# Optimization experiments

Hardware: AMD Instinct MI355X
Metric: run time of the kernel (lower is better)

## Reference

```python
import jax, jax.numpy as jnp
import numpy as np

B, N, D, STK_TOTAL = 8, 2048, 128, 4000


def setup_inputs() -> dict:
    key = jax.random.key(0)
    k1, k2, k3, k4 = jax.random.split(key, 4)
    x = jax.random.normal(k1, (B, N, D), dtype=jnp.float32)
    stk_ten = jax.random.randint(k2, (B, N), 0, STK_TOTAL, dtype=jnp.int32)
    # learned parameter tables (trained state; original inits: ones / xavier-uniform)
    stk_matrix = jax.random.normal(k3, (STK_TOTAL, STK_TOTAL), dtype=jnp.float32)
    stk_weight = jax.random.normal(k4, (STK_TOTAL, STK_TOTAL), dtype=jnp.float32)
    return {"x": x, "stk_ten": stk_ten, "stk_matrix": stk_matrix, "stk_weight": stk_weight}


def reference(x, stk_ten, stk_matrix, stk_weight):
    # x: [B, N, D]; stk_ten: [B, N] int ids < STK_TOTAL
    idx = stk_ten.astype(jnp.int32)
    # per-batch double gather -> [B, N, N] submatrices (vectorized index_select x2)
    M = stk_matrix[idx[:, :, None], idx[:, None, :]]          # [B, N, N]
    W = jnp.abs(stk_weight[idx[:, :, None], idx[:, None, :]])  # [B, N, N]
    n = idx.shape[1]
    eye = jnp.eye(n, dtype=bool)                               # diag removal mask
    M = jnp.where(eye, jnp.float32(0.0), M)                    # stk_m_s - diag_embed(diag)
    W = jnp.where(eye, jnp.float32(0.0), W)
    # dropout is identity in inference mode (training=False)
    att = jax.nn.softmax(W, axis=2)                            # [B, N, N]
    out = jnp.matmul(M * att, x)                               # [B, N, D]
    return out
```

## Files before the change

### kernel.cpp

```cpp
#include <hip/hip_runtime.h>
#include <hip/hip_fp16.h>
#include <math.h>

#define BATCH 8
#define N 2048
#define D 128
#define ST 4000

#define TJ 64
#define IT 16
#define KQ 4
#define TPW 8

typedef short bf16x8 __attribute__((ext_vector_type(8)));
typedef float f32x4  __attribute__((ext_vector_type(4)));
typedef unsigned u32x4 __attribute__((ext_vector_type(4)));

__device__ __forceinline__ unsigned short f2bf(float f) {
    union { float f; unsigned u; } v; v.f = f;
    const unsigned r = v.u + 0x7FFFu + ((v.u >> 16) & 1u);
    return (unsigned short)(r >> 16);
}

__global__ __launch_bounds__(256) void pack_kernel(
    const float* __restrict__ M, const float* __restrict__ W,
    unsigned* __restrict__ P)
{
    const size_t i4 = ((size_t)blockIdx.x * 256 + threadIdx.x) * 4;
    const f32x4 m4 = __builtin_nontemporal_load((const f32x4*)(M + i4));
    const f32x4 w4 = __builtin_nontemporal_load((const f32x4*)(W + i4));
    u32x4 o;
    {
        const float e = __expf(fabsf(w4.x));
        o.x = ((unsigned)f2bf(m4.x * e) << 16) | (unsigned)__half_as_ushort(__float2half(e));
    }
    {
        const float e = __expf(fabsf(w4.y));
        o.y = ((unsigned)f2bf(m4.y * e) << 16) | (unsigned)__half_as_ushort(__float2half(e));
    }
    {
        const float e = __expf(fabsf(w4.z));
        o.z = ((unsigned)f2bf(m4.z * e) << 16) | (unsigned)__half_as_ushort(__float2half(e));
    }
    {
        const float e = __expf(fabsf(w4.w));
        o.w = ((unsigned)f2bf(m4.w * e) << 16) | (unsigned)__half_as_ushort(__float2half(e));
    }
    *(u32x4*)(P + i4) = o;
}

__global__ __launch_bounds__(1024) void sort_kernel(
    const int* __restrict__ stk_ten,
    int* __restrict__ sval,
    int* __restrict__ spos)
{
    __shared__ int hist[4000];
    __shared__ int base[4000];
    __shared__ int wsum[16];
    const int b = blockIdx.x, t = threadIdx.x;
    const int lane = t & 63, wv = t >> 6;
    const int* idxb = stk_ten + b * N;

    for (int j = t; j < 4000; j += 1024) hist[j] = 0;
    __syncthreads();
    const int v0 = idxb[t], v1 = idxb[t + 1024];
    atomicAdd(&hist[v0], 1);
    atomicAdd(&hist[v1], 1);
    __syncthreads();

    int h[4], c[4], run = 0;
    #pragma unroll
    for (int i = 0; i < 4; ++i) {
        const int bi = 4 * t + i;
        h[i] = (bi < 4000) ? hist[bi] : 0;
        run += h[i];
        c[i] = run;
    }
    const int tsum = run;
    int incl = tsum;
    #pragma unroll
    for (int d = 1; d < 64; d <<= 1) {
        const int tmp = __shfl_up(incl, d, 64);
        if (lane >= d) incl += tmp;
    }
    if (lane == 63) wsum[wv] = incl;
    __syncthreads();
    if (t < 16) {
        const int v = wsum[t];
        int iv = v;
        #pragma unroll
        for (int d = 1; d < 16; d <<= 1) {
            const int tmp = __shfl_up(iv, d, 64);
            if (lane >= d) iv += tmp;
        }
        wsum[t] = iv - v;
    }
    __syncthreads();
    const int ex = incl - tsum + wsum[wv];
    #pragma unroll
    for (int i = 0; i < 4; ++i) {
        const int bi = 4 * t + i;
        if (bi < 4000) base[bi] = ex + c[i] - h[i];
    }
    __syncthreads();
    for (int j = t; j < 4000; j += 1024) hist[j] = 0;
    __syncthreads();
    {
        const int p0 = base[v0] + atomicAdd(&hist[v0], 1);
        sval[b * N + p0] = v0; spos[b * N + p0] = t;
        const int p1 = base[v1] + atomicAdd(&hist[v1], 1);
        sval[b * N + p1] = v1; spos[b * N + p1] = t + 1024;
    }
}

__global__ __launch_bounds__(256) void xt_kernel(
    const float* __restrict__ x,
    const int* __restrict__ spos,
    unsigned short* __restrict__ xT)
{
    __shared__ float xs[TJ][129];
    __shared__ int sp_s[TJ];
    const int t  = threadIdx.x;
    const int b  = blockIdx.x >> 5;
    const int jt = blockIdx.x & 31;
    const int j0 = jt * TJ;
    if (t < TJ) sp_s[t] = spos[b * N + j0 + t];
    __syncthreads();
    const int tx = t & 31, ty = t >> 5;
    const float* xb = x + (size_t)b * N * D;
    #pragma unroll
    for (int p = 0; p < 8; ++p) {
        const int r = ty + 8 * p;
        const float* src = xb + (size_t)sp_s[r] * D;
        #pragma unroll
        for (int i = 0; i < 4; ++i)
            xs[r][tx + 32 * i] = src[tx + 32 * i];
    }
    __syncthreads();
    const int jp = t & 31, dd0 = t >> 5;
    unsigned short* xTb = xT + (size_t)b * D * N;
    #pragma unroll
    for (int q = 0; q < 16; ++q) {
        const int dd = dd0 + 8 * q;
        const unsigned lo = f2bf(xs[2 * jp][dd]);
        const unsigned hi = f2bf(xs[2 * jp + 1][dd]);
        *(unsigned*)(xTb + (size_t)dd * N + j0 + 2 * jp) = (hi << 16) | lo;
    }
}

__global__ __launch_bounds__(256, 4) void fused_kernel(
    const unsigned short* __restrict__ xT,
    const int* __restrict__ stk_ten,
    const unsigned* __restrict__ P,
    const int* __restrict__ sval,
    const int* __restrict__ spos,
    float* __restrict__ out)
{
    __shared__ __align__(16) unsigned short cs[KQ][IT * 72];
    __shared__ float accs[IT][132];
    __shared__ float lbuf[KQ][IT];
    __shared__ int ri_s[IT];

    const int t    = threadIdx.x;
    const int lane = t & 63;
    const int w    = t >> 6;
    const int wg   = (blockIdx.x & 7) * 128 + (blockIdx.x >> 3);
    const int b    = wg >> 7;
    const int i0   = (wg & 127) * IT;

    if (t < IT) ri_s[t] = stk_ten[b * N + i0 + t];
    for (int z = t; z < IT * 132; z += 256) (&accs[0][0])[z] = 0.0f;
    __syncthreads();

    unsigned rowoff[IT];
    #pragma unroll
    for (int m = 0; m < IT; ++m) rowoff[m] = (unsigned)ri_s[m] * ST;

    const int* svb = sval + b * N;
    const int* spb = spos + b * N;
    const unsigned short* xTb = xT + (size_t)b * D * N;
    unsigned short* csw = &cs[w][0];

    f32x4 acc[8];
    #pragma unroll
    for (int nb = 0; nb < 8; ++nb)
        #pragma unroll
        for (int r = 0; r < 4; ++r) acc[nb][r] = 0.0f;
    float l_part[IT];
    #pragma unroll
    for (int m = 0; m < IT; ++m) l_part[m] = 0.0f;

    const int jbase = w * (TPW * TJ);
    const int brow  = lane & 15;
    const int bcol  = (lane >> 4) * 8;

    int cj = svb[jbase + lane];
    int pj = spb[jbase + lane];
    unsigned gv[IT];
    #pragma unroll
    for (int m = 0; m < IT; ++m) gv[m] = P[rowoff[m] + (unsigned)cj];

    for (int tt = 0; tt < TPW; ++tt) {
        const int j0  = jbase + tt * TJ;
        const int j0n = (tt == TPW - 1) ? jbase : j0 + TJ;

        const int cjn = svb[j0n + lane];
        const int pjn = spb[j0n + lane];
        uint4 bv[8];
        #pragma unroll
        for (int nb = 0; nb < 8; ++nb)
            bv[nb] = *(const uint4*)(xTb + (size_t)(nb * 16 + brow) * N + j0 + bcol);

        #pragma unroll
        for (int m = 0; m < IT; ++m) {
            const unsigned u = gv[m];
            const float e = __half2float(__ushort_as_half((unsigned short)(u & 0xFFFFu)));
            const bool diag = (pj == i0 + m);
            l_part[m] += diag ? 1.0f : e;
            csw[m * 72 + lane] = diag ? (unsigned short)0 : (unsigned short)(u >> 16);
        }

        const bf16x8 av0 = *(const bf16x8*)(csw + brow * 72 + bcol);
        const bf16x8 av1 = *(const bf16x8*)(csw + brow * 72 + 32 + bcol);

        unsigned gvn[IT];
        #pragma unroll
        for (int m = 0; m < IT; ++m) gvn[m] = P[rowoff[m] + (unsigned)cjn];

        #pragma unroll
        for (int nb = 0; nb < 8; ++nb)
            acc[nb] = __builtin_amdgcn_mfma_f32_16x16x32_bf16(
                av0, *(const bf16x8*)&bv[nb], acc[nb], 0, 0, 0);
        #pragma unroll
        for (int nb = 0; nb < 8; ++nb)
            bv[nb] = *(const uint4*)(xTb + (size_t)(nb * 16 + brow) * N + j0 + 32 + bcol);
        #pragma unroll
        for (int nb = 0; nb < 8; ++nb)
            acc[nb] = __builtin_amdgcn_mfma_f32_16x16x32_bf16(
                av1, *(const bf16x8*)&bv[nb], acc[nb], 0, 0, 0);

        #pragma unroll
        for (int m = 0; m < IT; ++m) gv[m] = gvn[m];
        cj = cjn; pj = pjn;
    }

    #pragma unroll
    for (int m = 0; m < IT; ++m) {
        float v = l_part[m];
        #pragma unroll
        for (int d = 1; d < 64; d <<= 1) v += __shfl_xor(v, d, 64);
        if (lane == 0) lbuf[w][m] = v;
    }
    #pragma unroll
    for (int nb = 0; nb < 8; ++nb)
        #pragma unroll
        for (int r = 0; r < 4; ++r)
            atomicAdd(&accs[(lane >> 4) * 4 + r][nb * 16 + (lane & 15)], acc[nb][r]);
    __syncthreads();

    #pragma unroll
    for (int rr = 0; rr < 4; ++rr) {
        const int row = 4 * w + rr;
        const float linv = 1.0f /
            (lbuf[0][row] + lbuf[1][row] + lbuf[2][row] + lbuf[3][row]);
        #pragma unroll
        for (int p = 0; p < 2; ++p) {
            const int dd = lane + 64 * p;
            out[((size_t)(b * N + i0 + row) << 7) + dd] = accs[row][dd] * linv;
        }
    }
}

extern "C" void kernel_launch(void* const* d_in, const int* in_sizes, int n_in,
                              void* d_out, int out_size, void* d_ws, size_t ws_size,
                              hipStream_t stream) {
    const float* x          = (const float*)d_in[0];
    const int*   stk_ten    = (const int*)d_in[1];
    const float* stk_matrix = (const float*)d_in[2];
    const float* stk_weight = (const float*)d_in[3];
    float* out = (float*)d_out;

    unsigned* P = (unsigned*)d_ws;
    int* sval = (int*)(P + (size_t)ST * ST);
    int* spos = sval + BATCH * N;
    unsigned short* xT = (unsigned short*)(spos + BATCH * N);

    pack_kernel<<<(ST * ST) / 1024, 256, 0, stream>>>(stk_matrix, stk_weight, P);
    sort_kernel<<<BATCH, 1024, 0, stream>>>(stk_ten, sval, spos);
    xt_kernel<<<BATCH * (N / TJ), 256, 0, stream>>>(x, spos, xT);
    fused_kernel<<<BATCH * (N / IT), 256, 0, stream>>>(
        xT, stk_ten, P, sval, spos, out);
}
```

Baseline: 275.1 us.

## Compute softmax denominators with MFMA and deepen gather prefetch pipeline

The exp weight is now packed as bf16 instead of fp16, so the per-row softmax denominator can be summed by an extra MFMA against a ones vector. This replaces the per-element scalar accumulation and the 16 cross-lane shuffle reductions. The index and gather loads are prefetched two tiles ahead, the row bases are made wave-uniform with readfirstlane, and the launch bounds are changed to an explicit waves-per-EU attribute. The cost is more LDS for the exp tile, more registers in flight, and lower precision for the denominator (bf16 instead of fp16).

```diff
diff --git a/kernel.cpp b/kernel.cpp
--- a/kernel.cpp
+++ b/kernel.cpp
@@ -32,19 +32,19 @@
     u32x4 o;
     {
         const float e = __expf(fabsf(w4.x));
-        o.x = ((unsigned)f2bf(m4.x * e) << 16) | (unsigned)__half_as_ushort(__float2half(e));
+        o.x = ((unsigned)f2bf(m4.x * e) << 16) | (unsigned)f2bf(e);
     }
     {
         const float e = __expf(fabsf(w4.y));
-        o.y = ((unsigned)f2bf(m4.y * e) << 16) | (unsigned)__half_as_ushort(__float2half(e));
+        o.y = ((unsigned)f2bf(m4.y * e) << 16) | (unsigned)f2bf(e);
     }
     {
         const float e = __expf(fabsf(w4.z));
-        o.z = ((unsigned)f2bf(m4.z * e) << 16) | (unsigned)__half_as_ushort(__float2half(e));
+        o.z = ((unsigned)f2bf(m4.z * e) << 16) | (unsigned)f2bf(e);
     }
     {
         const float e = __expf(fabsf(w4.w));
-        o.w = ((unsigned)f2bf(m4.w * e) << 16) | (unsigned)__half_as_ushort(__float2half(e));
+        o.w = ((unsigned)f2bf(m4.w * e) << 16) | (unsigned)f2bf(e);
     }
     *(u32x4*)(P + i4) = o;
 }
@@ -148,7 +148,8 @@
     }
 }
 
-__global__ __launch_bounds__(256, 4) void fused_kernel(
+__global__ __launch_bounds__(256) __attribute__((amdgpu_waves_per_eu(4, 4)))
+void fused_kernel(
     const unsigned short* __restrict__ xT,
     const int* __restrict__ stk_ten,
     const unsigned* __restrict__ P,
@@ -157,6 +158,7 @@
     float* __restrict__ out)
 {
     __shared__ __align__(16) unsigned short cs[KQ][IT * 72];
+    __shared__ __align__(16) unsigned short es[KQ][IT * 72];
     __shared__ float accs[IT][132];
     __shared__ float lbuf[KQ][IT];
     __shared__ int ri_s[IT];
@@ -172,40 +174,56 @@
     for (int z = t; z < IT * 132; z += 256) (&accs[0][0])[z] = 0.0f;
     __syncthreads();
 
-    unsigned rowoff[IT];
-    #pragma unroll
-    for (int m = 0; m < IT; ++m) rowoff[m] = (unsigned)ri_s[m] * ST;
+    unsigned rowbase[IT];
+    #pragma unroll
+    for (int m = 0; m < IT; ++m)
+        rowbase[m] = (unsigned)__builtin_amdgcn_readfirstlane(ri_s[m]) * (unsigned)ST;
 
     const int* svb = sval + b * N;
     const int* spb = spos + b * N;
     const unsigned short* xTb = xT + (size_t)b * D * N;
     unsigned short* csw = &cs[w][0];
+    unsigned short* esw = &es[w][0];
 
     f32x4 acc[8];
     #pragma unroll
     for (int nb = 0; nb < 8; ++nb)
         #pragma unroll
         for (int r = 0; r < 4; ++r) acc[nb][r] = 0.0f;
-    float l_part[IT];
-    #pragma unroll
-    for (int m = 0; m < IT; ++m) l_part[m] = 0.0f;
+    f32x4 accl;
+    #pragma unroll
+    for (int r = 0; r < 4; ++r) accl[r] = 0.0f;
+
+    bf16x8 onesv;
+    #pragma unroll
+    for (int k = 0; k < 8; ++k) onesv[k] = (short)0x3F80;
 
     const int jbase = w * (TPW * TJ);
     const int brow  = lane & 15;
     const int bcol  = (lane >> 4) * 8;
 
-    int cj = svb[jbase + lane];
-    int pj = spb[jbase + lane];
     unsigned gv[IT];
-    #pragma unroll
-    for (int m = 0; m < IT; ++m) gv[m] = P[rowoff[m] + (unsigned)cj];
+    int cjn, pj, pjn;
+    {
+        const int c0 = svb[jbase + lane];
+        pj  = spb[jbase + lane];
+        cjn = svb[jbase + TJ + lane];
+        pjn = spb[jbase + TJ + lane];
+        #pragma unroll
+        for (int m = 0; m < IT; ++m) gv[m] = P[rowbase[m] + (unsigned)c0];
+    }
 
     for (int tt = 0; tt < TPW; ++tt) {
-        const int j0  = jbase + tt * TJ;
-        const int j0n = (tt == TPW - 1) ? jbase : j0 + TJ;
-
-        const int cjn = svb[j0n + lane];
-        const int pjn = spb[j0n + lane];
+        const int j0 = jbase + tt * TJ;
+        const int j2 = (tt + 2 < TPW) ? j0 + 2 * TJ : jbase;
+
+        unsigned gvn[IT];
+        #pragma unroll
+        for (int m = 0; m < IT; ++m) gvn[m] = P[rowbase[m] + (unsigned)cjn];
+
+        const int cj2 = svb[j2 + lane];
+        const int pj2 = spb[j2 + lane];
+
         uint4 bv[8];
         #pragma unroll
         for (int nb = 0; nb < 8; ++nb)
@@ -214,23 +232,22 @@
         #pragma unroll
         for (int m = 0; m < IT; ++m) {
             const unsigned u = gv[m];
-            const float e = __half2float(__ushort_as_half((unsigned short)(u & 0xFFFFu)));
             const bool diag = (pj == i0 + m);
-            l_part[m] += diag ? 1.0f : e;
-            csw[m * 72 + lane] = diag ? (unsigned short)0 : (unsigned short)(u >> 16);
+            csw[m * 72 + lane] = diag ? (unsigned short)0      : (unsigned short)(u >> 16);
+            esw[m * 72 + lane] = diag ? (unsigned short)0x3F80 : (unsigned short)(u & 0xFFFFu);
         }
 
         const bf16x8 av0 = *(const bf16x8*)(csw + brow * 72 + bcol);
         const bf16x8 av1 = *(const bf16x8*)(csw + brow * 72 + 32 + bcol);
-
-        unsigned gvn[IT];
-        #pragma unroll
-        for (int m = 0; m < IT; ++m) gvn[m] = P[rowoff[m] + (unsigned)cjn];
+        const bf16x8 ae0 = *(const bf16x8*)(esw + brow * 72 + bcol);
+        const bf16x8 ae1 = *(const bf16x8*)(esw + brow * 72 + 32 + bcol);
 
         #pragma unroll
         for (int nb = 0; nb < 8; ++nb)
             acc[nb] = __builtin_amdgcn_mfma_f32_16x16x32_bf16(
                 av0, *(const bf16x8*)&bv[nb], acc[nb], 0, 0, 0);
+        accl = __builtin_amdgcn_mfma_f32_16x16x32_bf16(ae0, onesv, accl, 0, 0, 0);
+
         #pragma unroll
         for (int nb = 0; nb < 8; ++nb)
             bv[nb] = *(const uint4*)(xTb + (size_t)(nb * 16 + brow) * N + j0 + 32 + bcol);
@@ -238,18 +255,17 @@
         for (int nb = 0; nb < 8; ++nb)
             acc[nb] = __builtin_amdgcn_mfma_f32_16x16x32_bf16(
                 av1, *(const bf16x8*)&bv[nb], acc[nb], 0, 0, 0);
+        accl = __builtin_amdgcn_mfma_f32_16x16x32_bf16(ae1, onesv, accl, 0, 0, 0);
 
         #pragma unroll
         for (int m = 0; m < IT; ++m) gv[m] = gvn[m];
-        cj = cjn; pj = pjn;
-    }
-
-    #pragma unroll
-    for (int m = 0; m < IT; ++m) {
-        float v = l_part[m];
-        #pragma unroll
-        for (int d = 1; d < 64; d <<= 1) v += __shfl_xor(v, d, 64);
-        if (lane == 0) lbuf[w][m] = v;
+        pj = pjn; cjn = cj2; pjn = pj2;
+    }
+
+    if ((lane & 15) == 0) {
+        #pragma unroll
+        for (int r = 0; r < 4; ++r)
+            lbuf[w][(lane >> 4) * 4 + r] = accl[r];
     }
     #pragma unroll
     for (int nb = 0; nb < 8; ++nb)
```

Result: no change. 275.0 us (-0.0%).
